# Optimization experiments

Hardware: AMD Instinct MI355X
Metric: run time of the kernel (lower is better)

## Reference

```python
import jax, jax.numpy as jnp
import numpy as np

WS = 8            # window size
N = WS * WS       # tokens per window
C = 192           # in_features
H = 6             # heads
HD = C // H       # head dim
MH = 256          # meta network hidden
BW = 4096         # batch_size * windows
NW_MASK = 64      # number of mask window patterns


def _relative_coords_log():
    idx = np.arange(WS)
    coords = np.stack(np.meshgrid(idx, idx, indexing='ij'), axis=0).reshape(2, -1)  # [2, N]
    rel = coords[:, :, None] - coords[:, None, :]            # [2, N, N]
    rel = rel.transpose(1, 2, 0).reshape(-1, 2).astype(np.float32)  # [N*N, 2]
    return jnp.asarray(np.sign(rel) * np.log1p(np.abs(rel)))


def setup_inputs() -> dict:
    key = jax.random.key(0)
    ks = jax.random.split(key, 12)
    s = 0.02
    return {
        'x': jax.random.normal(ks[0], (BW, C, WS, WS), jnp.float32),
        'mask': jax.random.normal(ks[1], (NW_MASK, N, N), jnp.float32),
        'W_qkv': jax.random.normal(ks[2], (C, 3 * C), jnp.float32) * s,
        'b_qkv': jnp.zeros((3 * C,), jnp.float32),
        'W_proj': jax.random.normal(ks[3], (C, C), jnp.float32) * s,
        'b_proj': jnp.zeros((C,), jnp.float32),
        'mW1': jax.random.normal(ks[4], (2, MH), jnp.float32) * 0.1,
        'mb1': jnp.zeros((MH,), jnp.float32),
        'mW2': jax.random.normal(ks[5], (MH, H), jnp.float32) * 0.1,
        'mb2': jnp.zeros((H,), jnp.float32),
        'tau': jnp.ones((H,), jnp.float32),
    }


def _l2norm(v):
    n = jnp.sqrt(jnp.sum(v * v, axis=-1, keepdims=True))
    return v / jnp.maximum(n, 1e-12)


def reference(x, mask, W_qkv, b_qkv, W_proj, b_proj, mW1, mb1, mW2, mb2, tau):
    Bw = x.shape[0]
    # [Bw, C, ws, ws] -> tokens [Bw, N, C]
    tokens = x.reshape(Bw, C, N).transpose(0, 2, 1)
    qkv = tokens @ W_qkv + b_qkv                                  # [Bw, N, 3C]
    qkv = qkv.reshape(Bw, N, 3, H, HD).transpose(2, 0, 3, 1, 4)   # [3, Bw, H, N, HD]
    q, k, v = qkv[0], qkv[1], qkv[2]
    # scaled cosine attention
    attn = jnp.einsum('bhnd,bhmd->bhnm', _l2norm(q), _l2norm(k))
    attn = attn / jnp.clip(tau, 0.01, None)[None, :, None, None]
    # continuous relative position bias via meta network
    rel_log = _relative_coords_log()                              # [N*N, 2]
    bias = jax.nn.relu(rel_log @ mW1 + mb1) @ mW2 + mb2           # [N*N, H]
    bias = bias.T.reshape(H, N, N)
    attn = attn + bias[None]
    # shifted-window mask, pattern indexed by window id modulo nW_mask
    idx = jnp.arange(Bw) % mask.shape[0]
    attn = attn + mask[idx][:, None]                              # [Bw, 1, N, N]
    attn = jax.nn.softmax(attn, axis=-1)
    out = jnp.einsum('bhnm,bhmd->bhnd', attn, v)
    out = out.transpose(0, 2, 1, 3).reshape(Bw, N, C)
    out = out @ W_proj + b_proj
    # back to [Bw, C, ws, ws]
    return out.transpose(0, 2, 1).reshape(Bw, C, WS, WS)
```

## Files before the change

### kernel.cpp

```cpp
#include <hip/hip_runtime.h>

typedef _Float16 f16;
typedef _Float16 f16x2 __attribute__((ext_vector_type(2)));
typedef _Float16 f16x4 __attribute__((ext_vector_type(4)));
typedef _Float16 f16x8 __attribute__((ext_vector_type(8)));
typedef float f32x4 __attribute__((ext_vector_type(4)));

#define NT 64
#define CH 192
#define NH 6
#define MH 256
#define BWIN 4096
#define LOG2E 1.44269504f

#define STOK 200
#define SMEM_BYTES 49152

#define MFMA16(a, b, c) __builtin_amdgcn_mfma_f32_16x16x16f16(a, b, c, 0, 0, 0)
#define MFMA32(a, b, c) __builtin_amdgcn_mfma_f32_16x16x32_f16(a, b, c, 0, 0, 0)

__device__ __forceinline__ int qkidx(int n, int d) {
    return n * 32 + ((((d >> 3) + (n >> 1)) & 3) << 3) + (d & 7);
}

__global__ void bias_kernel(const float* __restrict__ mW1, const float* __restrict__ mb1,
                            const float* __restrict__ mW2, const float* __restrict__ mb2,
                            float* __restrict__ bias_tbl) {
    int p = blockIdx.x * blockDim.x + threadIdx.x;
    if (p >= NT * NT) return;
    int n = p >> 6, m = p & 63;
    float di = (float)((n >> 3) - (m >> 3));
    float dj = (float)((n & 7) - (m & 7));
    float r0 = copysignf(log1pf(fabsf(di)), di);
    float r1 = copysignf(log1pf(fabsf(dj)), dj);
    float acc[NH];
#pragma unroll
    for (int h = 0; h < NH; h++) acc[h] = mb2[h];
    for (int k = 0; k < MH; k++) {
        float hv = fmaxf(r0 * mW1[k] + r1 * mW1[MH + k] + mb1[k], 0.0f);
#pragma unroll
        for (int h = 0; h < NH; h++) acc[h] += hv * mW2[k * NH + h];
    }
#pragma unroll
    for (int h = 0; h < NH; h++) bias_tbl[h * (NT * NT) + p] = acc[h];
}

__global__ void prep_kernel(const float* __restrict__ Wqkv, const float* __restrict__ Wproj,
                            f16* __restrict__ Wpk, f16* __restrict__ Wpp) {
    int i = blockIdx.x * blockDim.x + threadIdx.x;
    const int NQ = 36 * 6 * 64 * 8;
    if (i < NQ) {
        int t = i & 7, lane = (i >> 3) & 63, ks = (i >> 9) % 6, ct = i >> 9; ct /= 6;
        int o = 16 * ct + (lane & 15);
        int c = ks * 32 + (lane >> 4) * 8 + t;
        Wpk[i] = (f16)Wqkv[c * 576 + o];
    } else if (i < NQ + 12 * 6 * 64 * 8) {
        int j = i - NQ;
        int t = j & 7, lane = (j >> 3) & 63, ks = (j >> 9) % 6, ct = j >> 9; ct /= 6;
        int o = 16 * ct + (lane & 15);
        int c = ks * 32 + (lane >> 4) * 8 + t;
        Wpp[j] = (f16)Wproj[c * 192 + o];
    }
}

__global__ void comb_kernel(const float* __restrict__ mask, const float* __restrict__ bias_tbl,
                            float* __restrict__ comb) {
    int j = blockIdx.x * blockDim.x + threadIdx.x;
    if (j >= 64 * NH * NT * NT) return;
    int im = j / (NH * NT * NT);
    int rem = j % (NH * NT * NT);
    int h = rem >> 12;
    int p = rem & 4095;
    comb[j] = (mask[im * 4096 + p] + bias_tbl[h * 4096 + p]) * LOG2E;
}

__launch_bounds__(384)
__global__ void attn_kernel(const float* __restrict__ x, const float* __restrict__ bqkv,
                            const float* __restrict__ bproj, const float* __restrict__ tau,
                            const f16* __restrict__ Wpk, const f16* __restrict__ Wpp,
                            const float* __restrict__ comb, float* __restrict__ out) {
    __shared__ __align__(16) char smem[SMEM_BYTES];
    f16* tok = (f16*)smem;
    f16* qk  = (f16*)smem;
    f16* ao  = (f16*)smem;

    const int b   = blockIdx.x;
    const int tid = threadIdx.x;
    const int l   = tid & 63;
    const int w   = __builtin_amdgcn_readfirstlane(tid >> 6);
    const int c16 = l & 15;
    const int g4  = l >> 4;

    {
        const float* xb = x + (size_t)b * (CH * NT);
        const int n4 = 4 * c16;
#pragma unroll
        for (int i = 0; i < 4; i++) {
            int c = 32 * w + 8 * g4 + 2 * i;
            f32x4 a0 = *(const f32x4*)(xb + c * NT + n4);
            f32x4 a1 = *(const f32x4*)(xb + (c + 1) * NT + n4);
#pragma unroll
            for (int j = 0; j < 4; j++) {
                f16x2 p;
                p[0] = (f16)a0[j];
                p[1] = (f16)a1[j];
                *(f16x2*)(tok + (n4 + j) * STOK + c) = p;
            }
        }
    }
    __syncthreads();

    f16x4 hq[2][4], hk[2][4];
    {
        f32x4 aq_[2][4] = {};
#pragma unroll
        for (int ks = 0; ks < 6; ks++) {
            f16x8 af[4];
#pragma unroll
            for (int nt = 0; nt < 4; nt++)
                af[nt] = *(const f16x8*)(tok + (16 * nt + c16) * STOK + ks * 32 + 8 * g4);
#pragma unroll
            for (int dt = 0; dt < 2; dt++) {
                f16x8 wf = *(const f16x8*)(Wpk + (((size_t)(2 * w + dt) * 6 + ks) * 64 + l) * 8);
#pragma unroll
                for (int nt = 0; nt < 4; nt++)
                    aq_[dt][nt] = MFMA32(wf, af[nt], aq_[dt][nt]);
            }
        }
#pragma unroll
        for (int dt = 0; dt < 2; dt++) {
            f32x4 bb = *(const f32x4*)(bqkv + 32 * w + 16 * dt + 4 * g4);
#pragma unroll
            for (int nt = 0; nt < 4; nt++)
#pragma unroll
                for (int r = 0; r < 4; r++) aq_[dt][nt][r] += bb[r];
        }
#pragma unroll
        for (int nt = 0; nt < 4; nt++) {
            float ss = 0.f;
#pragma unroll
            for (int dt = 0; dt < 2; dt++)
#pragma unroll
                for (int r = 0; r < 4; r++) ss += aq_[dt][nt][r] * aq_[dt][nt][r];
            ss += __shfl_xor(ss, 16);
            ss += __shfl_xor(ss, 32);
            float iq = 1.0f / fmaxf(sqrtf(ss), 1e-12f);
#pragma unroll
            for (int dt = 0; dt < 2; dt++)
#pragma unroll
                for (int r = 0; r < 4; r++) hq[dt][nt][r] = (f16)(aq_[dt][nt][r] * iq);
        }
    }
    {
        f32x4 ak_[2][4] = {};
#pragma unroll
        for (int ks = 0; ks < 6; ks++) {
            f16x8 af[4];
#pragma unroll
            for (int nt = 0; nt < 4; nt++)
                af[nt] = *(const f16x8*)(tok + (16 * nt + c16) * STOK + ks * 32 + 8 * g4);
#pragma unroll
            for (int dt = 0; dt < 2; dt++) {
                f16x8 wf = *(const f16x8*)(Wpk + (((size_t)(12 + 2 * w + dt) * 6 + ks) * 64 + l) * 8);
#pragma unroll
                for (int nt = 0; nt < 4; nt++)
                    ak_[dt][nt] = MFMA32(wf, af[nt], ak_[dt][nt]);
            }
        }
#pragma unroll
        for (int dt = 0; dt < 2; dt++) {
            f32x4 bb = *(const f32x4*)(bqkv + 192 + 32 * w + 16 * dt + 4 * g4);
#pragma unroll
            for (int nt = 0; nt < 4; nt++)
#pragma unroll
                for (int r = 0; r < 4; r++) ak_[dt][nt][r] += bb[r];
        }
#pragma unroll
        for (int nt = 0; nt < 4; nt++) {
            float ss = 0.f;
#pragma unroll
            for (int dt = 0; dt < 2; dt++)
#pragma unroll
                for (int r = 0; r < 4; r++) ss += ak_[dt][nt][r] * ak_[dt][nt][r];
            ss += __shfl_xor(ss, 16);
            ss += __shfl_xor(ss, 32);
            float ik = 1.0f / fmaxf(sqrtf(ss), 1e-12f);
#pragma unroll
            for (int dt = 0; dt < 2; dt++)
#pragma unroll
                for (int r = 0; r < 4; r++) hk[dt][nt][r] = (f16)(ak_[dt][nt][r] * ik);
        }
    }
    f16x4 vb[2][4];
    {
        f32x4 av_[2][4] = {};
#pragma unroll
        for (int ks = 0; ks < 6; ks++) {
            f16x8 af[4];
#pragma unroll
            for (int mt = 0; mt < 4; mt++)
                af[mt] = *(const f16x8*)(tok + (16 * mt + c16) * STOK + ks * 32 + 8 * g4);
#pragma unroll
            for (int dt = 0; dt < 2; dt++) {
                f16x8 wf = *(const f16x8*)(Wpk + (((size_t)(24 + 2 * w + dt) * 6 + ks) * 64 + l) * 8);
#pragma unroll
                for (int mt = 0; mt < 4; mt++)
                    av_[dt][mt] = MFMA32(af[mt], wf, av_[dt][mt]);
            }
        }
#pragma unroll
        for (int dt = 0; dt < 2; dt++) {
            float bb = bqkv[384 + 32 * w + 16 * dt + c16];
#pragma unroll
            for (int mt = 0; mt < 4; mt++)
#pragma unroll
                for (int r = 0; r < 4; r++) vb[dt][mt][r] = (f16)(av_[dt][mt][r] + bb);
        }
    }

    __syncthreads();

    f16* qh = qk + (w * 2 + 0) * 2048;
    f16* kh = qk + (w * 2 + 1) * 2048;
#pragma unroll
    for (int nt = 0; nt < 4; nt++)
#pragma unroll
        for (int dt = 0; dt < 2; dt++) {
            int base = qkidx(16 * nt + c16, 16 * dt + 4 * g4);
            f16x2 p;
            p[0] = hq[dt][nt][0]; p[1] = hq[dt][nt][1];
            *(f16x2*)(qh + base) = p;
            p[0] = hq[dt][nt][2]; p[1] = hq[dt][nt][3];
            *(f16x2*)(qh + base + 2) = p;
            p[0] = hk[dt][nt][0]; p[1] = hk[dt][nt][1];
            *(f16x2*)(kh + base) = p;
            p[0] = hk[dt][nt][2]; p[1] = hk[dt][nt][3];
            *(f16x2*)(kh + base + 2) = p;
        }

    f32x4 sv[4][4];
    {
        f16x8 aqf[4];
#pragma unroll
        for (int t = 0; t < 4; t++)
            aqf[t] = *(const f16x8*)(qh + qkidx(16 * t + c16, 8 * g4));
#pragma unroll
        for (int mt = 0; mt < 4; mt++) {
            f16x8 akf = *(const f16x8*)(kh + qkidx(16 * mt + c16, 8 * g4));
#pragma unroll
            for (int nt = 0; nt < 4; nt++) {
                f32x4 z = {};
                sv[mt][nt] = MFMA32(akf, aqf[nt], z);
            }
        }
    }

    {
        const float itau_l2 = LOG2E / fmaxf(tau[w], 0.01f);
        const float* cb = comb + ((size_t)((b & 63) * NH + w)) * (NT * NT);
#pragma unroll
        for (int mt = 0; mt < 4; mt++)
#pragma unroll
            for (int nt = 0; nt < 4; nt++) {
                f32x4 cc = *(const f32x4*)(cb + (16 * nt + c16) * NT + 16 * mt + 4 * g4);
#pragma unroll
                for (int r = 0; r < 4; r++)
                    sv[mt][nt][r] = sv[mt][nt][r] * itau_l2 + cc[r];
            }
    }

#pragma unroll
    for (int nt = 0; nt < 4; nt++) {
        float mx = sv[0][nt][0];
#pragma unroll
        for (int mt = 0; mt < 4; mt++)
#pragma unroll
            for (int r = 0; r < 4; r++) mx = fmaxf(mx, sv[mt][nt][r]);
        mx = fmaxf(mx, __shfl_xor(mx, 16));
        mx = fmaxf(mx, __shfl_xor(mx, 32));
        float sum = 0.f;
#pragma unroll
        for (int mt = 0; mt < 4; mt++)
#pragma unroll
            for (int r = 0; r < 4; r++) {
                float p = exp2f(sv[mt][nt][r] - mx);
                sv[mt][nt][r] = p;
                sum += p;
            }
        sum += __shfl_xor(sum, 16);
        sum += __shfl_xor(sum, 32);
        float ris = 1.0f / sum;
#pragma unroll
        for (int mt = 0; mt < 4; mt++)
#pragma unroll
            for (int r = 0; r < 4; r++) sv[mt][nt][r] *= ris;
    }

    f16x4 pa[4][4];
#pragma unroll
    for (int mk = 0; mk < 4; mk++)
#pragma unroll
        for (int nt = 0; nt < 4; nt++) {
            f16x4 h;
#pragma unroll
            for (int r = 0; r < 4; r++) h[r] = (f16)sv[mk][nt][r];
            pa[mk][nt] = h;
        }

    f32x4 av[4][2] = {};
#pragma unroll
    for (int mk = 0; mk < 4; mk++)
#pragma unroll
        for (int nt = 0; nt < 4; nt++)
#pragma unroll
            for (int dt = 0; dt < 2; dt++)
                av[nt][dt] = MFMA16(pa[mk][nt], vb[dt][mk], av[nt][dt]);

    __syncthreads();

#pragma unroll
    for (int nt = 0; nt < 4; nt++)
#pragma unroll
        for (int dt = 0; dt < 2; dt++)
#pragma unroll
            for (int r = 0; r < 4; r++)
                ao[(16 * nt + 4 * g4 + r) * STOK + 32 * w + 16 * dt + c16] = (f16)av[nt][dt][r];
    __syncthreads();

    f32x4 acc2[2][4] = {};
#pragma unroll
    for (int ks = 0; ks < 6; ks++) {
        f16x8 af[4];
#pragma unroll
        for (int rt = 0; rt < 4; rt++)
            af[rt] = *(const f16x8*)(ao + (16 * rt + c16) * STOK + ks * 32 + 8 * g4);
#pragma unroll
        for (int c2 = 0; c2 < 2; c2++) {
            f16x8 bw = *(const f16x8*)(Wpp + (((size_t)(2 * w + c2) * 6 + ks) * 64 + l) * 8);
#pragma unroll
            for (int rt = 0; rt < 4; rt++)
                acc2[c2][rt] = MFMA32(af[rt], bw, acc2[c2][rt]);
        }
    }
    float* ob = out + (size_t)b * (CH * NT);
#pragma unroll
    for (int c2 = 0; c2 < 2; c2++) {
        int c = 16 * (2 * w + c2) + c16;
        float bp = bproj[c];
#pragma unroll
        for (int rt = 0; rt < 4; rt++) {
            f32x4 o4 = acc2[c2][rt];
            o4[0] += bp; o4[1] += bp; o4[2] += bp; o4[3] += bp;
            *(f32x4*)(ob + c * NT + 16 * rt + 4 * g4) = o4;
        }
    }
}

#define WS_BIAS 0
#define WS_WPK  98304
#define WS_WPP  319488
#define WS_COMB 393216

extern "C" void kernel_launch(void* const* d_in, const int* in_sizes, int n_in,
                              void* d_out, int out_size, void* d_ws, size_t ws_size,
                              hipStream_t stream) {
    const float* x     = (const float*)d_in[0];
    const float* mask  = (const float*)d_in[1];
    const float* Wqkv  = (const float*)d_in[2];
    const float* bqkv  = (const float*)d_in[3];
    const float* Wproj = (const float*)d_in[4];
    const float* bproj = (const float*)d_in[5];
    const float* mW1   = (const float*)d_in[6];
    const float* mb1   = (const float*)d_in[7];
    const float* mW2   = (const float*)d_in[8];
    const float* mb2   = (const float*)d_in[9];
    const float* tau   = (const float*)d_in[10];

    char* ws = (char*)d_ws;
    float* bias_tbl = (float*)(ws + WS_BIAS);
    f16*   Wpk      = (f16*)(ws + WS_WPK);
    f16*   Wpp      = (f16*)(ws + WS_WPP);
    float* comb     = (float*)(ws + WS_COMB);

    bias_kernel<<<16, 256, 0, stream>>>(mW1, mb1, mW2, mb2, bias_tbl);
    int prep_n = 36 * 6 * 64 * 8 + 12 * 6 * 64 * 8;
    prep_kernel<<<(prep_n + 255) / 256, 256, 0, stream>>>(Wqkv, Wproj, Wpk, Wpp);
    int comb_n = 64 * NH * NT * NT;
    comb_kernel<<<(comb_n + 255) / 256, 256, 0, stream>>>(mask, bias_tbl, comb);
    attn_kernel<<<BWIN, 384, 0, stream>>>(x, bqkv, bproj, tau, Wpk, Wpp, comb,
                                          (float*)d_out);
}
```

Baseline: 338.4 us.

## Split fused attention into QKV-projection and attention kernels via workspace

Splits the single fused kernel into two. A QKV kernel writes L2-normalized q, k and raw v in f16 to a global workspace, and a second kernel runs attention and the output projection, processing query tiles in two halves. Each kernel uses less shared memory (about 25 KB versus 48 KB) and fewer live registers, so more blocks can be resident per CU. The cost is an extra round trip of roughly 300 MB of f16 QKV through HBM plus one more launch. The old fused path is kept as a fallback when the workspace is too small.

```diff
diff --git a/kernel.cpp b/kernel.cpp
--- a/kernel.cpp
+++ b/kernel.cpp
@@ -14,7 +14,8 @@
 #define LOG2E 1.44269504f
 
 #define STOK 200
-#define SMEM_BYTES 49152
+#define SMEM_FUSED 49152
+#define SMEM_SPLIT 25600
 
 #define MFMA16(a, b, c) __builtin_amdgcn_mfma_f32_16x16x16f16(a, b, c, 0, 0, 0)
 #define MFMA32(a, b, c) __builtin_amdgcn_mfma_f32_16x16x32_f16(a, b, c, 0, 0, 0)
@@ -75,11 +76,295 @@
 }
 
 __launch_bounds__(384)
-__global__ void attn_kernel(const float* __restrict__ x, const float* __restrict__ bqkv,
-                            const float* __restrict__ bproj, const float* __restrict__ tau,
-                            const f16* __restrict__ Wpk, const f16* __restrict__ Wpp,
-                            const float* __restrict__ comb, float* __restrict__ out) {
-    __shared__ __align__(16) char smem[SMEM_BYTES];
+__global__ void qkv_kernel(const float* __restrict__ x, const float* __restrict__ bqkv,
+                           const f16* __restrict__ Wpk, f16* __restrict__ qkv_ws) {
+    __shared__ __align__(16) f16 tok[NT * STOK];
+
+    const int tid = threadIdx.x;
+    const int l   = tid & 63;
+    const int w   = __builtin_amdgcn_readfirstlane(tid >> 6);
+    const int b   = blockIdx.x;
+    const int c16 = l & 15;
+    const int g4  = l >> 4;
+
+    {
+        const float* xb = x + (size_t)b * (CH * NT);
+        const int n4 = 4 * c16;
+#pragma unroll
+        for (int i = 0; i < 4; i++) {
+            int c = 32 * w + 8 * g4 + 2 * i;
+            f32x4 a0 = *(const f32x4*)(xb + c * NT + n4);
+            f32x4 a1 = *(const f32x4*)(xb + (c + 1) * NT + n4);
+#pragma unroll
+            for (int j = 0; j < 4; j++) {
+                f16x2 p;
+                p[0] = (f16)a0[j];
+                p[1] = (f16)a1[j];
+                *(f16x2*)(tok + (n4 + j) * STOK + c) = p;
+            }
+        }
+    }
+    __syncthreads();
+
+    f16* dstq = qkv_ws + (size_t)(b * NH + w) * 6144;
+    f16* dstk = dstq + 2048;
+    f16* dstv = dstq + 4096;
+
+    {
+        f32x4 acc[2][4] = {};
+#pragma unroll
+        for (int ks = 0; ks < 6; ks++) {
+            f16x8 af[4];
+#pragma unroll
+            for (int nt = 0; nt < 4; nt++)
+                af[nt] = *(const f16x8*)(tok + (16 * nt + c16) * STOK + ks * 32 + 8 * g4);
+#pragma unroll
+            for (int dt = 0; dt < 2; dt++) {
+                f16x8 wf = *(const f16x8*)(Wpk + (((size_t)(2 * w + dt) * 6 + ks) * 64 + l) * 8);
+#pragma unroll
+                for (int nt = 0; nt < 4; nt++)
+                    acc[dt][nt] = MFMA32(wf, af[nt], acc[dt][nt]);
+            }
+        }
+        f32x4 bb0 = *(const f32x4*)(bqkv + 32 * w + 4 * g4);
+        f32x4 bb1 = *(const f32x4*)(bqkv + 32 * w + 16 + 4 * g4);
+#pragma unroll
+        for (int nt = 0; nt < 4; nt++) {
+            float a0[4], a1[4];
+            float ss = 0.f;
+#pragma unroll
+            for (int r = 0; r < 4; r++) {
+                a0[r] = acc[0][nt][r] + bb0[r];
+                a1[r] = acc[1][nt][r] + bb1[r];
+                ss += a0[r] * a0[r] + a1[r] * a1[r];
+            }
+            ss += __shfl_xor(ss, 16);
+            ss += __shfl_xor(ss, 32);
+            float inv = 1.0f / fmaxf(sqrtf(ss), 1e-12f);
+            f16x4 h0, h1;
+#pragma unroll
+            for (int r = 0; r < 4; r++) {
+                h0[r] = (f16)(a0[r] * inv);
+                h1[r] = (f16)(a1[r] * inv);
+            }
+            *(f16x4*)(dstq + (16 * nt + c16) * 32 + 4 * g4)      = h0;
+            *(f16x4*)(dstq + (16 * nt + c16) * 32 + 16 + 4 * g4) = h1;
+        }
+    }
+    {
+        f32x4 acc[2][4] = {};
+#pragma unroll
+        for (int ks = 0; ks < 6; ks++) {
+            f16x8 af[4];
+#pragma unroll
+            for (int nt = 0; nt < 4; nt++)
+                af[nt] = *(const f16x8*)(tok + (16 * nt + c16) * STOK + ks * 32 + 8 * g4);
+#pragma unroll
+            for (int dt = 0; dt < 2; dt++) {
+                f16x8 wf = *(const f16x8*)(Wpk + (((size_t)(12 + 2 * w + dt) * 6 + ks) * 64 + l) * 8);
+#pragma unroll
+                for (int nt = 0; nt < 4; nt++)
+                    acc[dt][nt] = MFMA32(wf, af[nt], acc[dt][nt]);
+            }
+        }
+        f32x4 bb0 = *(const f32x4*)(bqkv + CH + 32 * w + 4 * g4);
+        f32x4 bb1 = *(const f32x4*)(bqkv + CH + 32 * w + 16 + 4 * g4);
+#pragma unroll
+        for (int nt = 0; nt < 4; nt++) {
+            float a0[4], a1[4];
+            float ss = 0.f;
+#pragma unroll
+            for (int r = 0; r < 4; r++) {
+                a0[r] = acc[0][nt][r] + bb0[r];
+                a1[r] = acc[1][nt][r] + bb1[r];
+                ss += a0[r] * a0[r] + a1[r] * a1[r];
+            }
+            ss += __shfl_xor(ss, 16);
+            ss += __shfl_xor(ss, 32);
+            float inv = 1.0f / fmaxf(sqrtf(ss), 1e-12f);
+            f16x4 h0, h1;
+#pragma unroll
+            for (int r = 0; r < 4; r++) {
+                h0[r] = (f16)(a0[r] * inv);
+                h1[r] = (f16)(a1[r] * inv);
+            }
+            *(f16x4*)(dstk + (16 * nt + c16) * 32 + 4 * g4)      = h0;
+            *(f16x4*)(dstk + (16 * nt + c16) * 32 + 16 + 4 * g4) = h1;
+        }
+    }
+    {
+        f32x4 acc[2][4] = {};
+#pragma unroll
+        for (int ks = 0; ks < 6; ks++) {
+            f16x8 af[4];
+#pragma unroll
+            for (int mt = 0; mt < 4; mt++)
+                af[mt] = *(const f16x8*)(tok + (16 * mt + c16) * STOK + ks * 32 + 8 * g4);
+#pragma unroll
+            for (int dt = 0; dt < 2; dt++) {
+                f16x8 wf = *(const f16x8*)(Wpk + (((size_t)(24 + 2 * w + dt) * 6 + ks) * 64 + l) * 8);
+#pragma unroll
+                for (int mt = 0; mt < 4; mt++)
+                    acc[dt][mt] = MFMA32(af[mt], wf, acc[dt][mt]);
+            }
+        }
+#pragma unroll
+        for (int dt = 0; dt < 2; dt++) {
+            float bb = bqkv[384 + 32 * w + 16 * dt + c16];
+#pragma unroll
+            for (int mt = 0; mt < 4; mt++) {
+                f16x4 h;
+#pragma unroll
+                for (int r = 0; r < 4; r++) h[r] = (f16)(acc[dt][mt][r] + bb);
+                *(f16x4*)(dstv + ((dt * 4 + mt) * 64 + l) * 4) = h;
+            }
+        }
+    }
+}
+
+__launch_bounds__(384)
+__global__ void attn2_kernel(const float* __restrict__ tau, const f16* __restrict__ Wpp,
+                             const float* __restrict__ bproj, const float* __restrict__ comb,
+                             const f16* __restrict__ qkv_ws, float* __restrict__ out) {
+    __shared__ __align__(16) f16 ao[NT * STOK];
+
+    const int tid = threadIdx.x;
+    const int l   = tid & 63;
+    const int w   = __builtin_amdgcn_readfirstlane(tid >> 6);
+    const int b   = blockIdx.x;
+    const int c16 = l & 15;
+    const int g4  = l >> 4;
+
+    const f16* qg = qkv_ws + (size_t)(b * NH + w) * 6144;
+    const f16* kg = qg + 2048;
+    const f16* vg = qg + 4096;
+
+    f16x4 vb[2][4];
+#pragma unroll
+    for (int dt = 0; dt < 2; dt++)
+#pragma unroll
+        for (int mk = 0; mk < 4; mk++)
+            vb[dt][mk] = *(const f16x4*)(vg + ((dt * 4 + mk) * 64 + l) * 4);
+
+    const float itau_l2 = LOG2E / fmaxf(tau[w], 0.01f);
+    const float* cb = comb + ((size_t)((b & 63) * NH + w)) * (NT * NT);
+
+#pragma unroll
+    for (int half = 0; half < 2; half++) {
+        f16x8 aqf[2];
+#pragma unroll
+        for (int ntl = 0; ntl < 2; ntl++)
+            aqf[ntl] = *(const f16x8*)(qg + (16 * (2 * half + ntl) + c16) * 32 + 8 * g4);
+        f32x4 sv[4][2];
+#pragma unroll
+        for (int mt = 0; mt < 4; mt++) {
+            f16x8 akf = *(const f16x8*)(kg + (16 * mt + c16) * 32 + 8 * g4);
+#pragma unroll
+            for (int ntl = 0; ntl < 2; ntl++) {
+                f32x4 z = {};
+                sv[mt][ntl] = MFMA32(akf, aqf[ntl], z);
+            }
+        }
+#pragma unroll
+        for (int mt = 0; mt < 4; mt++)
+#pragma unroll
+            for (int ntl = 0; ntl < 2; ntl++) {
+                int nt = 2 * half + ntl;
+                f32x4 cc = *(const f32x4*)(cb + (16 * nt + c16) * NT + 16 * mt + 4 * g4);
+#pragma unroll
+                for (int r = 0; r < 4; r++)
+                    sv[mt][ntl][r] = sv[mt][ntl][r] * itau_l2 + cc[r];
+            }
+#pragma unroll
+        for (int ntl = 0; ntl < 2; ntl++) {
+            float mx = sv[0][ntl][0];
+#pragma unroll
+            for (int mt = 0; mt < 4; mt++)
+#pragma unroll
+                for (int r = 0; r < 4; r++) mx = fmaxf(mx, sv[mt][ntl][r]);
+            mx = fmaxf(mx, __shfl_xor(mx, 16));
+            mx = fmaxf(mx, __shfl_xor(mx, 32));
+            float sum = 0.f;
+#pragma unroll
+            for (int mt = 0; mt < 4; mt++)
+#pragma unroll
+                for (int r = 0; r < 4; r++) {
+                    float p = exp2f(sv[mt][ntl][r] - mx);
+                    sv[mt][ntl][r] = p;
+                    sum += p;
+                }
+            sum += __shfl_xor(sum, 16);
+            sum += __shfl_xor(sum, 32);
+            float ris = 1.0f / sum;
+#pragma unroll
+            for (int mt = 0; mt < 4; mt++)
+#pragma unroll
+                for (int r = 0; r < 4; r++) sv[mt][ntl][r] *= ris;
+        }
+        f16x4 pa[4][2];
+#pragma unroll
+        for (int mk = 0; mk < 4; mk++)
+#pragma unroll
+            for (int ntl = 0; ntl < 2; ntl++) {
+                f16x4 h;
+#pragma unroll
+                for (int r = 0; r < 4; r++) h[r] = (f16)sv[mk][ntl][r];
+                pa[mk][ntl] = h;
+            }
+        f32x4 av[2][2] = {};
+#pragma unroll
+        for (int mk = 0; mk < 4; mk++)
+#pragma unroll
+            for (int ntl = 0; ntl < 2; ntl++)
+#pragma unroll
+                for (int dt = 0; dt < 2; dt++)
+                    av[ntl][dt] = MFMA16(pa[mk][ntl], vb[dt][mk], av[ntl][dt]);
+#pragma unroll
+        for (int ntl = 0; ntl < 2; ntl++)
+#pragma unroll
+            for (int dt = 0; dt < 2; dt++)
+#pragma unroll
+                for (int r = 0; r < 4; r++)
+                    ao[(16 * (2 * half + ntl) + 4 * g4 + r) * STOK + 32 * w + 16 * dt + c16] =
+                        (f16)av[ntl][dt][r];
+    }
+    __syncthreads();
+
+    f32x4 acc2[2][4] = {};
+#pragma unroll
+    for (int ks = 0; ks < 6; ks++) {
+        f16x8 af[4];
+#pragma unroll
+        for (int rt = 0; rt < 4; rt++)
+            af[rt] = *(const f16x8*)(ao + (16 * rt + c16) * STOK + ks * 32 + 8 * g4);
+#pragma unroll
+        for (int c2 = 0; c2 < 2; c2++) {
+            f16x8 bw = *(const f16x8*)(Wpp + (((size_t)(2 * w + c2) * 6 + ks) * 64 + l) * 8);
+#pragma unroll
+            for (int rt = 0; rt < 4; rt++)
+                acc2[c2][rt] = MFMA32(af[rt], bw, acc2[c2][rt]);
+        }
+    }
+    float* ob = out + (size_t)b * (CH * NT);
+#pragma unroll
+    for (int c2 = 0; c2 < 2; c2++) {
+        int c = 16 * (2 * w + c2) + c16;
+        float bp = bproj[c];
+#pragma unroll
+        for (int rt = 0; rt < 4; rt++) {
+            f32x4 o4 = acc2[c2][rt];
+            o4[0] += bp; o4[1] += bp; o4[2] += bp; o4[3] += bp;
+            *(f32x4*)(ob + c * NT + 16 * rt + 4 * g4) = o4;
+        }
+    }
+}
+
+__launch_bounds__(384)
+__global__ void attn_fused_kernel(const float* __restrict__ x, const float* __restrict__ bqkv,
+                                  const float* __restrict__ bproj, const float* __restrict__ tau,
+                                  const f16* __restrict__ Wpk, const f16* __restrict__ Wpp,
+                                  const float* __restrict__ comb, float* __restrict__ out) {
+    __shared__ __align__(16) char smem[SMEM_FUSED];
     f16* tok = (f16*)smem;
     f16* qk  = (f16*)smem;
     f16* ao  = (f16*)smem;
@@ -217,7 +502,6 @@
                 for (int r = 0; r < 4; r++) vb[dt][mt][r] = (f16)(av_[dt][mt][r] + bb);
         }
     }
-
     __syncthreads();
 
     f16* qh = qk + (w * 2 + 0) * 2048;
@@ -227,15 +511,10 @@
 #pragma unroll
         for (int dt = 0; dt < 2; dt++) {
             int base = qkidx(16 * nt + c16, 16 * dt + 4 * g4);
-            f16x2 p;
-            p[0] = hq[dt][nt][0]; p[1] = hq[dt][nt][1];
-            *(f16x2*)(qh + base) = p;
-            p[0] = hq[dt][nt][2]; p[1] = hq[dt][nt][3];
-            *(f16x2*)(qh + base + 2) = p;
-            p[0] = hk[dt][nt][0]; p[1] = hk[dt][nt][1];
-            *(f16x2*)(kh + base) = p;
-            p[0] = hk[dt][nt][2]; p[1] = hk[dt][nt][3];
-            *(f16x2*)(kh + base + 2) = p;
+            *(f16x2*)(qh + base)     = f16x2{hq[dt][nt][0], hq[dt][nt][1]};
+            *(f16x2*)(qh + base + 2) = f16x2{hq[dt][nt][2], hq[dt][nt][3]};
+            *(f16x2*)(kh + base)     = f16x2{hk[dt][nt][0], hk[dt][nt][1]};
+            *(f16x2*)(kh + base + 2) = f16x2{hk[dt][nt][2], hk[dt][nt][3]};
         }
 
     f32x4 sv[4][4];
@@ -254,7 +533,6 @@
             }
         }
     }
-
     {
         const float itau_l2 = LOG2E / fmaxf(tau[w], 0.01f);
         const float* cb = comb + ((size_t)((b & 63) * NH + w)) * (NT * NT);
@@ -268,7 +546,6 @@
                     sv[mt][nt][r] = sv[mt][nt][r] * itau_l2 + cc[r];
             }
     }
-
 #pragma unroll
     for (int nt = 0; nt < 4; nt++) {
         float mx = sv[0][nt][0];
@@ -295,7 +572,6 @@
 #pragma unroll
             for (int r = 0; r < 4; r++) sv[mt][nt][r] *= ris;
     }
-
     f16x4 pa[4][4];
 #pragma unroll
     for (int mk = 0; mk < 4; mk++)
@@ -306,7 +582,6 @@
             for (int r = 0; r < 4; r++) h[r] = (f16)sv[mk][nt][r];
             pa[mk][nt] = h;
         }
-
     f32x4 av[4][2] = {};
 #pragma unroll
     for (int mk = 0; mk < 4; mk++)
@@ -317,7 +592,6 @@
                 av[nt][dt] = MFMA16(pa[mk][nt], vb[dt][mk], av[nt][dt]);
 
     __syncthreads();
-
 #pragma unroll
     for (int nt = 0; nt < 4; nt++)
 #pragma unroll
@@ -360,6 +634,8 @@
 #define WS_WPK  98304
 #define WS_WPP  319488
 #define WS_COMB 393216
+#define WS_QKV  6684672
+#define WS_NEED ((size_t)WS_QKV + (size_t)BWIN * NH * 6144 * 2)
 
 extern "C" void kernel_launch(void* const* d_in, const int* in_sizes, int n_in,
                               void* d_out, int out_size, void* d_ws, size_t ws_size,
@@ -381,12 +657,19 @@
     f16*   Wpk      = (f16*)(ws + WS_WPK);
     f16*   Wpp      = (f16*)(ws + WS_WPP);
     float* comb     = (float*)(ws + WS_COMB);
+    f16*   qkv_ws   = (f16*)(ws + WS_QKV);
 
     bias_kernel<<<16, 256, 0, stream>>>(mW1, mb1, mW2, mb2, bias_tbl);
     int prep_n = 36 * 6 * 64 * 8 + 12 * 6 * 64 * 8;
     prep_kernel<<<(prep_n + 255) / 256, 256, 0, stream>>>(Wqkv, Wproj, Wpk, Wpp);
     int comb_n = 64 * NH * NT * NT;
     comb_kernel<<<(comb_n + 255) / 256, 256, 0, stream>>>(mask, bias_tbl, comb);
-    attn_kernel<<<BWIN, 384, 0, stream>>>(x, bqkv, bproj, tau, Wpk, Wpp, comb,
-                                          (float*)d_out);
-}
+
+    if (ws_size >= WS_NEED) {
+        qkv_kernel<<<BWIN, 384, 0, stream>>>(x, bqkv, Wpk, qkv_ws);
+        attn2_kernel<<<BWIN, 384, 0, stream>>>(tau, Wpp, bproj, comb, qkv_ws, (float*)d_out);
+    } else {
+        attn_fused_kernel<<<BWIN, 384, 0, stream>>>(x, bqkv, bproj, tau, Wpk, Wpp, comb,
+                                                    (float*)d_out);
+    }
+}
```

After: 330.3 us. 2.4% less time.
